# Optimization experiments

Measured on AMD Instinct MI355X. Metric: run time of the kernel, lower is better.

The kernel has to match this reference:

```python
import jax, jax.numpy as jnp
from jax import lax
import numpy as np

L, G, C = 4, 2, 4  # num_blocks, num_sparsity_groups, num_sparsity_cardinals
IMAGE_MEAN = 0.5
SCALE = 2


def _wn(v, g):
    # weight_norm over dims (1,2,3), g per output channel
    n = jnp.sqrt(jnp.sum(v * v, axis=(1, 2, 3), keepdims=True))
    return (g.reshape(-1, 1, 1, 1) / n) * v


def _conv(x, w, b, pad):
    y = lax.conv_general_dilated(x, w, (1, 1), [(pad, pad), (pad, pad)],
                                 dimension_numbers=('NCHW', 'OIHW', 'NCHW'))
    return y + b[None, :, None, None]


def _dyn_conv(x, v, g, b, mw, mb):
    # sparsity-routed conv: per-sample expert mixture of kernels
    w = _wn(v, g)                                   # [G*out, in, k, k]
    B = x.shape[0]
    logits = x.mean((-1, -2)) @ mw.T + mb           # [B, G*C]
    s = jax.nn.softmax(logits.reshape(B, G, C), axis=1)
    wv = w.reshape(G, C, -1, *w.shape[1:])          # [G, C, D, in, k, k]
    wper = jnp.einsum('bgc,gcdikl->bcdikl', s, wv)
    wper = wper.reshape(B, -1, *w.shape[1:])        # [B, out, in, k, k]
    bper = jnp.einsum('bgc,gcd->bcd', s, b.reshape(G, C, -1)).reshape(B, -1)

    def per_sample(xi, wi, bi):
        yi = lax.conv_general_dilated(xi[None], wi, (1, 1), [(1, 1), (1, 1)],
                                      dimension_numbers=('NCHW', 'OIHW', 'NCHW'))[0]
        return yi + bi[:, None, None]

    return jax.vmap(per_sample)(x, wper, bper)


def _pixel_shuffle(x, r):
    B, Cc, H, W = x.shape
    x = x.reshape(B, Cc // (r * r), r, r, H, W)
    x = x.transpose(0, 1, 4, 2, 5, 3)
    return x.reshape(B, Cc // (r * r), H * r, W * r)


def setup_inputs() -> dict:
    key = jax.random.key(0)
    ks = jax.random.split(key, 16)
    f32 = jnp.float32
    inp = {
        'x': jax.random.uniform(ks[0], (8, 3, 64, 64), dtype=f32),
        'head_v': jax.random.normal(ks[1], (64, 3, 3, 3), dtype=f32) * 0.05,
        'head_g': jnp.ones((64,), f32),
        'head_b': jnp.zeros((64,), f32),
        'b1_v': jax.random.normal(ks[2], (L, 512, 64, 3, 3), dtype=f32) * 0.05,
        'b1_g': jnp.full((L, 512), 2.0, f32),
        'b1_b': jnp.zeros((L, 512), f32),
        'b1_mw': jax.random.normal(ks[3], (L, 8, 64), dtype=f32) * 0.05,
        'b1_mb': jax.random.normal(ks[4], (L, 8), dtype=f32) * 0.05,
        'b2_v': jax.random.normal(ks[5], (L, 128, 256, 3, 3), dtype=f32) * 0.05,
        'b2_g': jnp.full((L, 128), 1.0 / np.sqrt(L), f32),
        'b2_b': jnp.zeros((L, 128), f32),
        'b2_mw': jax.random.normal(ks[6], (L, 8, 256), dtype=f32) * 0.05,
        'b2_mb': jax.random.normal(ks[7], (L, 8), dtype=f32) * 0.05,
        'tail_v': jax.random.normal(ks[8], (12, 64, 3, 3), dtype=f32) * 0.05,
        'tail_g': jnp.ones((12,), f32),
        'tail_b': jnp.zeros((12,), f32),
        'skip_v': jax.random.normal(ks[9], (12, 3, 5, 5), dtype=f32) * 0.05,
        'skip_g': jnp.ones((12,), f32),
        'skip_b': jnp.zeros((12,), f32),
    }
    return inp


def reference(x, head_v, head_g, head_b,
              b1_v, b1_g, b1_b, b1_mw, b1_mb,
              b2_v, b2_g, b2_b, b2_mw, b2_mb,
              tail_v, tail_g, tail_b,
              skip_v, skip_g, skip_b):
    x = x - IMAGE_MEAN
    h = _conv(x, _wn(head_v, head_g), head_b, pad=1)
    for l in range(L):
        r0 = h
        t = _dyn_conv(h, b1_v[l], b1_g[l], b1_b[l], b1_mw[l], b1_mb[l])
        t = jax.nn.relu(t)
        t = _dyn_conv(t, b2_v[l], b2_g[l], b2_b[l], b2_mw[l], b2_mb[l])
        h = t + r0
    body = _conv(h, _wn(tail_v, tail_g), tail_b, pad=1)
    s = _conv(x, _wn(skip_v, skip_g), skip_b, pad=2)
    y = _pixel_shuffle(body + s, SCALE) + IMAGE_MEAN
    return y
```

## Files before the change

kernel.cpp:

```cpp
#include <hip/hip_runtime.h>

typedef __attribute__((ext_vector_type(8))) short bf16x8;
typedef __attribute__((ext_vector_type(4))) float f32x4;
typedef __attribute__((ext_vector_type(4))) unsigned short u16x4;
typedef __attribute__((ext_vector_type(8))) unsigned short u16x8;

__device__ __forceinline__ unsigned short bf16u(float x) {
    unsigned int u = __builtin_bit_cast(unsigned int, x);
    unsigned int r = (u + 0x7fffu + ((u >> 16) & 1u)) >> 16;
    return (unsigned short)r;
}
__device__ __forceinline__ void gll16(const void* g, void* l) {
    __builtin_amdgcn_global_load_lds((const __attribute__((address_space(1))) void*)g,
                                     (__attribute__((address_space(3))) void*)l, 16, 0, 0);
}

__global__ __launch_bounds__(256) void zero_all(unsigned short* __restrict__ hbf,
                                                unsigned short* __restrict__ tbf,
                                                float* __restrict__ sums) {
    int i = blockIdx.x * 256 + threadIdx.x;
    u16x8 z8 = {0, 0, 0, 0, 0, 0, 0, 0};
    if (i < 16640) {
        int chv = i & 7, pb = i >> 3, pos = pb % 260, b = pb / 260;
        int y, x;
        if (pos < 66) { y = 0; x = pos; }
        else if (pos < 132) { y = 65; x = pos - 66; }
        else if (pos < 196) { y = pos - 131; x = 0; }
        else { y = pos - 195; x = 65; }
        *(u16x8*)&hbf[(((size_t)b * 66 + y) * 66 + x) * 64 + chv * 8] = z8;
    } else if (i < 83200) {
        int j = i - 16640;
        int chv = j & 31, pb = j >> 5, pos = pb % 260, b = pb / 260;
        int y, x;
        if (pos < 66) { y = 0; x = pos; }
        else if (pos < 132) { y = 65; x = pos - 66; }
        else if (pos < 196) { y = pos - 131; x = 0; }
        else { y = pos - 195; x = 65; }
        *(u16x8*)&tbf[(((size_t)b * 66 + y) * 66 + x) * 256 + chv * 8] = z8;
    } else {
        int k = i - 83200;
        f32x4 z4 = {0.f, 0.f, 0.f, 0.f};
        ((f32x4*)sums)[k] = z4;
    }
}

__global__ __launch_bounds__(256) void wn_all(
    const float* __restrict__ hv, const float* __restrict__ hg, float* __restrict__ hw,
    const float* __restrict__ tv, const float* __restrict__ tg, float* __restrict__ tw,
    const float* __restrict__ kv, const float* __restrict__ kg, float* __restrict__ kw,
    const float* __restrict__ b1v, const float* __restrict__ b1g, float* __restrict__ b1s,
    const float* __restrict__ b2v, const float* __restrict__ b2g, float* __restrict__ b2s) {
    int blk = blockIdx.x;
    const float *v, *g;
    float *outw = nullptr, *outs = nullptr;
    int len, row;
    if (blk < 64)        { v = hv;  g = hg;  outw = hw;  len = 27;   row = blk; }
    else if (blk < 76)   { v = tv;  g = tg;  outw = tw;  len = 576;  row = blk - 64; }
    else if (blk < 88)   { v = kv;  g = kg;  outw = kw;  len = 75;   row = blk - 76; }
    else if (blk < 2136) { v = b1v; g = b1g; outs = b1s; len = 576;  row = blk - 88; }
    else                 { v = b2v; g = b2g; outs = b2s; len = 2304; row = blk - 2136; }

    __shared__ float red[4];
    __shared__ float s_sc;
    const float* vr = v + (size_t)row * len;
    float ss = 0.f;
    for (int i = threadIdx.x; i < len; i += 256) { float a = vr[i]; ss += a * a; }
    for (int o = 32; o > 0; o >>= 1) ss += __shfl_down(ss, o);
    if ((threadIdx.x & 63) == 0) red[threadIdx.x >> 6] = ss;
    __syncthreads();
    if (threadIdx.x == 0) s_sc = g[row] / sqrtf(red[0] + red[1] + red[2] + red[3]);
    __syncthreads();
    float sc = s_sc;
    if (outs) {
        if (threadIdx.x == 0) outs[row] = sc;
    } else {
        float* orow = outw + (size_t)row * len;
        for (int i = threadIdx.x; i < len; i += 256) orow[i] = vr[i] * sc;
    }
}

__global__ __launch_bounds__(256) void combine_w2(
    const float* __restrict__ v, const float* __restrict__ scale,
    const float* __restrict__ msum, const float* __restrict__ mw,
    const float* __restrict__ mb, float* __restrict__ s_out,
    unsigned short* __restrict__ wq, int D, int IC, int OC, int MT, int icr) {
    __shared__ float lg[8];
    __shared__ float sv8[8];
    int tid = threadIdx.x;
    int bpb = (OC * IC * 9) >> 8;
    int b = blockIdx.x / bpb;
    {
        int j = tid >> 5, l32 = tid & 31;
        float part = 0.f;
        for (int i = l32; i < icr; i += 32) part += msum[b * icr + i] * mw[j * icr + i];
        for (int m = 16; m > 0; m >>= 1) part += __shfl_xor(part, m);
        if (l32 == 0) lg[j] = part * (1.f / 4096.f) + mb[j];
    }
    __syncthreads();
    if (tid < 8) {
        int g = tid >> 2, c = tid & 3;
        float l0 = lg[c], l1 = lg[4 + c];
        float m = fmaxf(l0, l1);
        float e0 = __expf(l0 - m), e1 = __expf(l1 - m);
        float val = ((g == 0) ? e0 : e1) / (e0 + e1);
        sv8[tid] = val;
        if (blockIdx.x == b * bpb) s_out[b * 8 + tid] = val;
    }
    __syncthreads();

    int idx = blockIdx.x * 256 + tid;
    int kj = idx & 7;
    int tmp = idx >> 3;
    int mo = tmp % MT; tmp /= MT;
    int kg = tmp & 3; tmp >>= 2;
    int t = tmp % 9; tmp /= 9;
    int KCh = IC >> 5;
    int kc = tmp % KCh; tmp /= KCh;
    int OT = OC / MT;
    int ot = tmp % OT;
    int oc = ot * MT + mo;
    int ic = kc * 32 + kg * 8 + kj;
    int c = oc / D;
    float s0 = sv8[c], s1 = sv8[4 + c];
    float val = s0 * scale[oc] * v[((size_t)oc * IC + ic) * 9 + t] +
                s1 * scale[OC + oc] * v[((size_t)(OC + oc) * IC + ic) * 9 + t];
    wq[idx] = bf16u(val);
}

__global__ void tail_repack(const float* __restrict__ tw, unsigned short* __restrict__ wq) {
    int idx = blockIdx.x * 256 + threadIdx.x;
    int kj = idx & 7;
    int tmp = idx >> 3;
    int mo = tmp % 16; tmp /= 16;
    int kg = tmp & 3; tmp >>= 2;
    int t = tmp % 9; tmp /= 9;
    int kc = tmp;
    int ic = kc * 32 + kg * 8 + kj;
    float val = (mo < 12) ? tw[((size_t)mo * 64 + ic) * 9 + t] : 0.f;
    wq[idx] = bf16u(val);
}

template <int IC, int OC, int MT, int WM, int WN, int NR,
          bool RELU, bool RES, bool WF32, bool WBF, int OCR, bool DYNB>
__global__ __launch_bounds__(256) void conv_mfma(
    const unsigned short* __restrict__ in_bf,
    const unsigned short* __restrict__ wq,
    const float* __restrict__ bias_raw, const float* __restrict__ s8, int lgD,
    const float* __restrict__ res, float* __restrict__ out,
    unsigned short* __restrict__ out_bf, float* __restrict__ msum, long wstride) {
    constexpr int KCH = IC / 32;
    constexpr int NRH = NR + 2;
    constexpr int NT = NR * 64;
    constexpr int NF = (NT / 16) / WN;
    constexpr int MW = MT / (16 * WM);
    constexpr int WELEM = 9 * 32 * MT;
    constexpr int SCH = NRH * 66 * 4;
    constexpr int WCH = WELEM / 8;

    __shared__ __align__(16) unsigned short S[NRH * 66 * 32];
    __shared__ __align__(16) unsigned short W[WELEM];
    __shared__ float MRED[WN][MT];

    const int b = blockIdx.z, ot = blockIdx.y;
    const int y0 = blockIdx.x * NR;
    const int tid = threadIdx.x;
    const int lane = tid & 63, wid = tid >> 6;
    const int wm = wid / WN, wn = wid % WN;
    const int l15 = lane & 15, lk = lane >> 4;
    const int wmo = wm * (MT / WM);
    const int wno = wn * (NT / WN);

    f32x4 acc[MW][NF];
#pragma unroll
    for (int mf = 0; mf < MW; ++mf)
#pragma unroll
        for (int nf = 0; nf < NF; ++nf)
#pragma unroll
            for (int q = 0; q < 4; ++q) acc[mf][nf][q] = 0.f;

    const unsigned short* inb = in_bf + (size_t)b * 66 * 66 * IC;
    const unsigned short* wqb = wq + (size_t)b * wstride + (size_t)ot * (KCH * WELEM);

    for (int kc = 0; kc < KCH; ++kc) {
        __syncthreads();
        const unsigned short* wsrc = wqb + kc * WELEM;
        for (int cb = wid; cb * 64 < WCH; cb += 4) {
            int p = cb * 64 + lane;
            if (p < WCH) gll16(wsrc + p * 8, (char*)W + p * 16);
        }
        const int icb = kc * 32;
        for (int cb = wid; cb * 64 < SCH; cb += 4) {
            int p = cb * 64 + lane;
            if (p < SCH) {
                int Lz = p ^ ((p >> 3) & 7);
                int lk2 = Lz & 3;
                int cr = Lz >> 2;
                int col = cr % 66, row = cr / 66;
                const unsigned short* src =
                    inb + ((size_t)(y0 + row) * 66 + col) * IC + icb + lk2 * 8;
                gll16(src, (char*)S + p * 16);
            }
        }
        __syncthreads();
#pragma unroll
        for (int t = 0; t < 9; ++t) {
            const int dy = t / 3, dx = t % 3;
            bf16x8 a[MW];
#pragma unroll
            for (int mf = 0; mf < MW; ++mf)
                a[mf] = *(const bf16x8*)&W[((t * 4 + lk) * MT + wmo + mf * 16 + l15) * 8];
#pragma unroll
            for (int nf = 0; nf < NF; ++nf) {
                int n = wno + nf * 16 + l15;
                int r = n >> 6, c = n & 63;
                int L = ((r + dy) * 66 + (c + dx)) * 4 + lk;
                int P = L ^ ((L >> 3) & 7);
                bf16x8 bv = *(const bf16x8*)((const char*)S + P * 16);
#pragma unroll
                for (int mf = 0; mf < MW; ++mf)
                    acc[mf][nf] = __builtin_amdgcn_mfma_f32_16x16x32_bf16(a[mf], bv, acc[mf][nf], 0, 0, 0);
            }
        }
    }

    float msr[MW][4];
#pragma unroll
    for (int mf = 0; mf < MW; ++mf) {
        int ocb = ot * MT + wmo + mf * 16 + lk * 4;
        float bv[4];
#pragma unroll
        for (int q = 0; q < 4; ++q) {
            int oc = ocb + q;
            bv[q] = 0.f;
            if (oc < OCR) {
                if (DYNB) {
                    int c = oc >> lgD;
                    bv[q] = s8[b * 8 + c] * bias_raw[oc] + s8[b * 8 + 4 + c] * bias_raw[OCR + oc];
                } else {
                    bv[q] = bias_raw[oc];
                }
            }
            msr[mf][q] = 0.f;
        }
#pragma unroll
        for (int nf = 0; nf < NF; ++nf) {
            int n = wno + nf * 16 + l15;
            int y = y0 + (n >> 6), x = n & 63;
            float vv[4];
#pragma unroll
            for (int q = 0; q < 4; ++q) {
                int oc = ocb + q;
                float v = 0.f;
                if (oc < OCR) {
                    v = acc[mf][nf][q] + bv[q];
                    if (RELU) v = fmaxf(v, 0.f);
                    size_t o = (((size_t)b * OCR + oc) * 64 + y) * 64 + x;
                    if (RES) v += res[o];
                    if (WF32) out[o] = v;
                    msr[mf][q] += v;
                }
                vv[q] = v;
            }
            if (WBF) {
                u16x4 pk;
#pragma unroll
                for (int q = 0; q < 4; ++q) pk[q] = bf16u(vv[q]);
                if (ocb < OCR)
                    *(u16x4*)&out_bf[(((size_t)b * 66 + y + 1) * 66 + (x + 1)) * OCR + ocb] = pk;
            }
        }
    }
    if (msum) {
#pragma unroll
        for (int mf = 0; mf < MW; ++mf)
#pragma unroll
            for (int q = 0; q < 4; ++q) {
                float vq = msr[mf][q];
                vq += __shfl_xor(vq, 1);
                vq += __shfl_xor(vq, 2);
                vq += __shfl_xor(vq, 4);
                vq += __shfl_xor(vq, 8);
                if (l15 == 0) MRED[wn][wmo + mf * 16 + lk * 4 + q] = vq;
            }
        __syncthreads();
        if (tid < MT) {
            float tot = 0.f;
#pragma unroll
            for (int w2 = 0; w2 < WN; ++w2) tot += MRED[w2][tid];
            atomicAdd(&msum[b * OCR + ot * MT + tid], tot);
        }
    }
}

__global__ __launch_bounds__(256) void head_conv(
    const float* __restrict__ in, const float* __restrict__ w,
    const float* __restrict__ bias, float* __restrict__ out,
    unsigned short* __restrict__ out_bf, float* __restrict__ hsum0) {
    constexpr int OCT = 16, IC = 3;
    __shared__ float s_in[34 * 34];
    __shared__ float s_w[OCT * 9];
    __shared__ float wred[4][OCT];
    int b = blockIdx.z;
    int ocBase = blockIdx.y * OCT;
    int ty0 = (blockIdx.x >> 1) * 32;
    int tx0 = (blockIdx.x & 1) * 32;
    int tid = threadIdx.x;
    int lane = tid & 63, wid = tid >> 6;
    int tx = tid & 15, ty = tid >> 4;

    float acc[OCT][4];
#pragma unroll
    for (int oc = 0; oc < OCT; ++oc)
#pragma unroll
        for (int p = 0; p < 4; ++p) acc[oc][p] = 0.f;

    const float* inb = in + (size_t)b * IC * 4096;
    for (int ic = 0; ic < IC; ++ic) {
        const float* src = inb + (size_t)ic * 4096;
        for (int i = tid; i < 34 * 34; i += 256) {
            int r = i / 34, cc = i % 34;
            int gy = ty0 + r - 1, gx = tx0 + cc - 1;
            float val = 0.f;
            if (gy >= 0 && gy < 64 && gx >= 0 && gx < 64) val = src[gy * 64 + gx] - 0.5f;
            s_in[i] = val;
        }
        for (int i = tid; i < OCT * 9; i += 256) {
            int oc = i / 9, t = i % 9;
            s_w[i] = w[((size_t)(ocBase + oc) * IC + ic) * 9 + t];
        }
        __syncthreads();
        float v[4][4];
#pragma unroll
        for (int r = 0; r < 4; ++r)
#pragma unroll
            for (int cc = 0; cc < 4; ++cc) v[r][cc] = s_in[(2 * ty + r) * 34 + (2 * tx + cc)];
#pragma unroll
        for (int oc = 0; oc < OCT; ++oc) {
#pragma unroll
            for (int ky = 0; ky < 3; ++ky)
#pragma unroll
                for (int kx = 0; kx < 3; ++kx) {
                    float wv = s_w[oc * 9 + ky * 3 + kx];
                    acc[oc][0] += wv * v[ky][kx];
                    acc[oc][1] += wv * v[ky][kx + 1];
                    acc[oc][2] += wv * v[ky + 1][kx];
                    acc[oc][3] += wv * v[ky + 1][kx + 1];
                }
        }
        __syncthreads();
    }
    int py = ty0 + 2 * ty, px = tx0 + 2 * tx;
#pragma unroll
    for (int oc = 0; oc < OCT; ++oc) {
        int og = ocBase + oc;
        float bv = bias[og];
        float osum = 0.f;
#pragma unroll
        for (int p = 0; p < 4; ++p) {
            int dy = p >> 1, dx = p & 1;
            float val = acc[oc][p] + bv;
            osum += val;
            out[(((size_t)b * 64 + og) * 64 + py + dy) * 64 + px + dx] = val;
            out_bf[(((size_t)b * 66 + py + dy + 1) * 66 + (px + dx + 1)) * 64 + og] = bf16u(val);
        }
        for (int m = 1; m < 64; m <<= 1) osum += __shfl_xor(osum, m);
        if (lane == 0) wred[wid][oc] = osum;
    }
    __syncthreads();
    if (tid < OCT)
        atomicAdd(&hsum0[b * 64 + ocBase + tid],
                  wred[0][tid] + wred[1][tid] + wred[2][tid] + wred[3][tid]);
}

__global__ __launch_bounds__(256) void shuffle_skip(
    const float* __restrict__ body, const float* __restrict__ x,
    const float* __restrict__ skw, const float* __restrict__ skb,
    float* __restrict__ out) {
    __shared__ float w[900];
    __shared__ float bb[12];
    int tid = threadIdx.x;
    for (int i = tid; i < 900; i += 256) w[i] = skw[i];
    if (tid < 12) bb[tid] = skb[tid];
    __syncthreads();
    int idx = blockIdx.x * 256 + tid;
    int ox = idx & 127;
    int oy = (idx >> 7) & 127;
    int v = idx >> 14;
    int c = v % 3;
    int b = v / 3;
    int rx = ox & 1, ry = oy & 1;
    int xx = ox >> 1, yy = oy >> 1;
    int ch = c * 4 + ry * 2 + rx;
    float acc = bb[ch];
    for (int ic = 0; ic < 3; ++ic)
        for (int ky = 0; ky < 5; ++ky) {
            int gy = yy + ky - 2;
            if (gy < 0 || gy >= 64) continue;
            for (int kx = 0; kx < 5; ++kx) {
                int gx = xx + kx - 2;
                if (gx < 0 || gx >= 64) continue;
                acc += w[((ch * 3 + ic) * 5 + ky) * 5 + kx] *
                       (x[((size_t)(b * 3 + ic) * 64 + gy) * 64 + gx] - 0.5f);
            }
        }
    size_t src = (((size_t)b * 12 + ch) * 64 + yy) * 64 + xx;
    out[idx] = body[src] + acc + 0.5f;
}

extern "C" void kernel_launch(void* const* d_in, const int* in_sizes, int n_in,
                              void* d_out, int out_size, void* d_ws, size_t ws_size,
                              hipStream_t stream) {
    const float* x      = (const float*)d_in[0];
    const float* head_v = (const float*)d_in[1];
    const float* head_g = (const float*)d_in[2];
    const float* head_b = (const float*)d_in[3];
    const float* b1_v   = (const float*)d_in[4];
    const float* b1_g   = (const float*)d_in[5];
    const float* b1_b   = (const float*)d_in[6];
    const float* b1_mw  = (const float*)d_in[7];
    const float* b1_mb  = (const float*)d_in[8];
    const float* b2_v   = (const float*)d_in[9];
    const float* b2_g   = (const float*)d_in[10];
    const float* b2_b   = (const float*)d_in[11];
    const float* b2_mw  = (const float*)d_in[12];
    const float* b2_mb  = (const float*)d_in[13];
    const float* tail_v = (const float*)d_in[14];
    const float* tail_g = (const float*)d_in[15];
    const float* tail_b = (const float*)d_in[16];
    const float* skip_v = (const float*)d_in[17];
    const float* skip_g = (const float*)d_in[18];
    const float* skip_b = (const float*)d_in[19];

    float* ws = (float*)d_ws;
    size_t off = 0;
    auto alloc = [&](size_t n) { float* p = ws + off; off += (n + 3) & ~(size_t)3; return p; };
    float* head_w = alloc(64 * 27);
    float* tail_w = alloc(12 * 576);
    float* skip_w = alloc(12 * 75);
    float* b1_sc  = alloc(2048);
    float* b2_sc  = alloc(512);
    float* h      = alloc((size_t)8 * 64 * 4096);
    float* sums   = alloc(10240);
    float* sbuf   = alloc(64);
    float* body   = alloc((size_t)8 * 12 * 4096);
    unsigned short* wq1  = (unsigned short*)alloc((size_t)8 * 256 * 576 / 2);
    unsigned short* wq2  = (unsigned short*)alloc((size_t)8 * 64 * 2304 / 2);
    unsigned short* wqt  = (unsigned short*)alloc(9216 / 2);
    unsigned short* h_bf = (unsigned short*)alloc((size_t)8 * 66 * 66 * 64 / 2);
    unsigned short* t_bf = (unsigned short*)alloc((size_t)8 * 66 * 66 * 256 / 2);
    (void)ws_size; (void)in_sizes; (void)n_in; (void)out_size;

    auto hsum = [&](int l) { return sums + l * 512; };
    auto tsum = [&](int l) { return sums + 2048 + l * 2048; };

    zero_all<<<335, 256, 0, stream>>>(h_bf, t_bf, sums);
    wn_all<<<2648, 256, 0, stream>>>(head_v, head_g, head_w, tail_v, tail_g, tail_w,
                                     skip_v, skip_g, skip_w, b1_v, b1_g, b1_sc,
                                     b2_v, b2_g, b2_sc);
    head_conv<<<dim3(4, 4, 8), 256, 0, stream>>>(x, head_w, head_b, h, h_bf, hsum(0));
    tail_repack<<<36, 256, 0, stream>>>(tail_w, wqt);

    for (int l = 0; l < 4; ++l) {
        combine_w2<<<4608, 256, 0, stream>>>(b1_v + (size_t)l * 512 * 576,
                                             b1_sc + (size_t)l * 512, hsum(l),
                                             b1_mw + (size_t)l * 8 * 64, b1_mb + l * 8,
                                             sbuf, wq1, 64, 64, 256, 64, 64);
        conv_mfma<64, 256, 64, 1, 4, 4, true, false, false, true, 256, true>
            <<<dim3(16, 4, 8), 256, 0, stream>>>(h_bf, wq1, b1_b + (size_t)l * 512, sbuf, 6,
                                                 nullptr, nullptr, t_bf, tsum(l), 147456);
        combine_w2<<<4608, 256, 0, stream>>>(b2_v + (size_t)l * 128 * 2304,
                                             b2_sc + (size_t)l * 128, tsum(l),
                                             b2_mw + (size_t)l * 8 * 256, b2_mb + l * 8,
                                             sbuf, wq2, 16, 256, 64, 32, 256);
        conv_mfma<256, 64, 32, 2, 2, 2, false, true, true, true, 64, true>
            <<<dim3(32, 2, 8), 256, 0, stream>>>(t_bf, wq2, b2_b + (size_t)l * 128, sbuf, 4,
                                                 h, h, h_bf, (l < 3) ? hsum(l + 1) : nullptr,
                                                 147456);
    }

    conv_mfma<64, 16, 16, 1, 4, 4, false, false, true, false, 12, false>
        <<<dim3(16, 1, 8), 256, 0, stream>>>(h_bf, wqt, tail_b, nullptr, 0,
                                             nullptr, body, nullptr, nullptr, 0);
    shuffle_skip<<<1536, 256, 0, stream>>>(body, x, skip_w, skip_b, (float*)d_out);
}
```

Before: 351.1 us.

## Double-buffer conv staging, block activations by 64 channels, rewrite weight combine

The conv kernel now stages the next K-chunk of weights and inputs into a second LDS buffer while the current chunk feeds the MFMAs, leaving one barrier per chunk instead of two. Intermediate activations are stored as 64-channel blocks so each K-chunk reads a compact region. The weight-combine kernel caches the needed weight rows in shared memory and writes packed 8-element bf16 vectors instead of one scalar per thread. The second conv uses a 64-channel output tile with one tile in the OC dimension. The cost is roughly double LDS use, which lowers occupancy, and fewer blocks for the second conv.

```diff
diff --git a/kernel.cpp b/kernel.cpp
--- a/kernel.cpp
+++ b/kernel.cpp
@@ -30,13 +30,14 @@
         *(u16x8*)&hbf[(((size_t)b * 66 + y) * 66 + x) * 64 + chv * 8] = z8;
     } else if (i < 83200) {
         int j = i - 16640;
-        int chv = j & 31, pb = j >> 5, pos = pb % 260, b = pb / 260;
+        int chv = j & 7, pb = j >> 3;
+        int pos = pb % 260, bc = pb / 260;
         int y, x;
         if (pos < 66) { y = 0; x = pos; }
         else if (pos < 132) { y = 65; x = pos - 66; }
         else if (pos < 196) { y = pos - 131; x = 0; }
         else { y = pos - 195; x = 65; }
-        *(u16x8*)&tbf[(((size_t)b * 66 + y) * 66 + x) * 256 + chv * 8] = z8;
+        *(u16x8*)&tbf[(((size_t)bc * 66 + y) * 66 + x) * 64 + chv * 8] = z8;
     } else {
         int k = i - 83200;
         f32x4 z4 = {0.f, 0.f, 0.f, 0.f};
@@ -79,22 +80,30 @@
     }
 }
 
-__global__ __launch_bounds__(256) void combine_w2(
+template <int IC, int GOC, int LGG>
+__global__ __launch_bounds__(256) void combine_v2(
     const float* __restrict__ v, const float* __restrict__ scale,
     const float* __restrict__ msum, const float* __restrict__ mw,
     const float* __restrict__ mb, float* __restrict__ s_out,
-    unsigned short* __restrict__ wq, int D, int IC, int OC, int MT, int icr) {
-    __shared__ float lg[8];
-    __shared__ float sv8[8];
+    unsigned short* __restrict__ wq, int D, int OC) {
+    constexpr int ROWF = IC * 9;
+    constexpr int KCh = IC / 32;
+    constexpr int TOTC = GOC * KCh * 9 * 4;
+    __shared__ float lv[2 * GOC * ROWF];
+    __shared__ float lg[8], sv8[8];
     int tid = threadIdx.x;
-    int bpb = (OC * IC * 9) >> 8;
-    int b = blockIdx.x / bpb;
+    int b = blockIdx.y, ocg = blockIdx.x * GOC;
     {
         int j = tid >> 5, l32 = tid & 31;
         float part = 0.f;
-        for (int i = l32; i < icr; i += 32) part += msum[b * icr + i] * mw[j * icr + i];
+        for (int i = l32; i < IC; i += 32) part += msum[b * IC + i] * mw[j * IC + i];
         for (int m = 16; m > 0; m >>= 1) part += __shfl_xor(part, m);
         if (l32 == 0) lg[j] = part * (1.f / 4096.f) + mb[j];
+    }
+    for (int i = tid; i < 2 * GOC * ROWF; i += 256) {
+        int r = i / ROWF, jj = i - r * ROWF;
+        int oc_r = (r / GOC) * OC + ocg + (r % GOC);
+        lv[i] = v[(size_t)oc_r * ROWF + jj] * scale[oc_r];
     }
     __syncthreads();
     if (tid < 8) {
@@ -104,27 +113,29 @@
         float e0 = __expf(l0 - m), e1 = __expf(l1 - m);
         float val = ((g == 0) ? e0 : e1) / (e0 + e1);
         sv8[tid] = val;
-        if (blockIdx.x == b * bpb) s_out[b * 8 + tid] = val;
-    }
-    __syncthreads();
-
-    int idx = blockIdx.x * 256 + tid;
-    int kj = idx & 7;
-    int tmp = idx >> 3;
-    int mo = tmp % MT; tmp /= MT;
-    int kg = tmp & 3; tmp >>= 2;
-    int t = tmp % 9; tmp /= 9;
-    int KCh = IC >> 5;
-    int kc = tmp % KCh; tmp /= KCh;
-    int OT = OC / MT;
-    int ot = tmp % OT;
-    int oc = ot * MT + mo;
-    int ic = kc * 32 + kg * 8 + kj;
-    int c = oc / D;
-    float s0 = sv8[c], s1 = sv8[4 + c];
-    float val = s0 * scale[oc] * v[((size_t)oc * IC + ic) * 9 + t] +
-                s1 * scale[OC + oc] * v[((size_t)(OC + oc) * IC + ic) * 9 + t];
-    wq[idx] = bf16u(val);
+        if (blockIdx.x == 0) s_out[b * 8 + tid] = val;
+    }
+    __syncthreads();
+    for (int ci = tid; ci < TOTC; ci += 256) {
+        int ml = ci & (GOC - 1);
+        int c = ci >> LGG;
+        int kg = c & 3, c2 = c >> 2;
+        int t = c2 % 9, kc = c2 / 9;
+        int oc = ocg + ml;
+        int cd = oc / D;
+        float s0 = sv8[cd], s1 = sv8[4 + cd];
+        const float* p0 = &lv[(size_t)ml * ROWF];
+        const float* p1 = &lv[(size_t)(GOC + ml) * ROWF];
+        u16x8 pk;
+#pragma unroll
+        for (int kj = 0; kj < 8; ++kj) {
+            int ic9 = (kc * 32 + kg * 8 + kj) * 9 + t;
+            pk[kj] = bf16u(s0 * p0[ic9] + s1 * p1[ic9]);
+        }
+        int ot = oc >> 6, mo = oc & 63;
+        size_t w_off = ((((size_t)(b * (OC >> 6) + ot) * KCh + kc) * 9 + t) * 4 + kg) * 512 + mo * 8;
+        *(u16x8*)&wq[w_off] = pk;
+    }
 }
 
 __global__ void tail_repack(const float* __restrict__ tw, unsigned short* __restrict__ wq) {
@@ -154,17 +165,20 @@
     constexpr int NF = (NT / 16) / WN;
     constexpr int MW = MT / (16 * WM);
     constexpr int WELEM = 9 * 32 * MT;
-    constexpr int SCH = NRH * 66 * 4;
+    constexpr int SELEM = NRH * 66 * 32;
     constexpr int WCH = WELEM / 8;
-
-    __shared__ __align__(16) unsigned short S[NRH * 66 * 32];
-    __shared__ __align__(16) unsigned short W[WELEM];
+    constexpr int SCH = SELEM / 8;
+    constexpr int OCB = (OCR % 64 == 0) ? OCR / 64 : 1;
+
+    __shared__ __align__(16) unsigned short S[2][SELEM];
+    __shared__ __align__(16) unsigned short W[2][WELEM];
     __shared__ float MRED[WN][MT];
 
     const int b = blockIdx.z, ot = blockIdx.y;
     const int y0 = blockIdx.x * NR;
     const int tid = threadIdx.x;
-    const int lane = tid & 63, wid = tid >> 6;
+    const int lane = tid & 63;
+    const int wid = tid >> 6;
     const int wm = wid / WN, wn = wid % WN;
     const int l15 = lane & 15, lk = lane >> 4;
     const int wmo = wm * (MT / WM);
@@ -178,49 +192,49 @@
 #pragma unroll
             for (int q = 0; q < 4; ++q) acc[mf][nf][q] = 0.f;
 
-    const unsigned short* inb = in_bf + (size_t)b * 66 * 66 * IC;
+    const unsigned short* inb = in_bf + (size_t)b * (IC / 64) * 4356 * 64;
     const unsigned short* wqb = wq + (size_t)b * wstride + (size_t)ot * (KCH * WELEM);
 
+    auto STAGE = [&](int kc, int buf) {
+        const unsigned short* wsrc = wqb + (size_t)kc * WELEM;
+        for (int i = tid; i < WCH; i += 256)
+            gll16(wsrc + i * 8, (char*)W[buf] + i * 16);
+        const unsigned short* sb = inb + (size_t)(kc >> 1) * (4356 * 64) + (kc & 1) * 32;
+        for (int i = tid; i < SCH; i += 256) {
+            int Lz = i ^ ((i >> 3) & 7);
+            int lk2 = Lz & 3, cr = Lz >> 2;
+            int col = cr % 66, row = cr / 66;
+            gll16(sb + ((size_t)(y0 + row) * 66 + col) * 64 + lk2 * 8,
+                  (char*)S[buf] + i * 16);
+        }
+    };
+
+    STAGE(0, 0);
+    __syncthreads();
     for (int kc = 0; kc < KCH; ++kc) {
-        __syncthreads();
-        const unsigned short* wsrc = wqb + kc * WELEM;
-        for (int cb = wid; cb * 64 < WCH; cb += 4) {
-            int p = cb * 64 + lane;
-            if (p < WCH) gll16(wsrc + p * 8, (char*)W + p * 16);
-        }
-        const int icb = kc * 32;
-        for (int cb = wid; cb * 64 < SCH; cb += 4) {
-            int p = cb * 64 + lane;
-            if (p < SCH) {
-                int Lz = p ^ ((p >> 3) & 7);
-                int lk2 = Lz & 3;
-                int cr = Lz >> 2;
-                int col = cr % 66, row = cr / 66;
-                const unsigned short* src =
-                    inb + ((size_t)(y0 + row) * 66 + col) * IC + icb + lk2 * 8;
-                gll16(src, (char*)S + p * 16);
-            }
-        }
-        __syncthreads();
+        if (kc + 1 < KCH) STAGE(kc + 1, (kc + 1) & 1);
+        const unsigned short* Sb = S[kc & 1];
+        const unsigned short* Wb = W[kc & 1];
 #pragma unroll
         for (int t = 0; t < 9; ++t) {
             const int dy = t / 3, dx = t % 3;
             bf16x8 a[MW];
 #pragma unroll
             for (int mf = 0; mf < MW; ++mf)
-                a[mf] = *(const bf16x8*)&W[((t * 4 + lk) * MT + wmo + mf * 16 + l15) * 8];
+                a[mf] = *(const bf16x8*)&Wb[((t * 4 + lk) * MT + wmo + mf * 16 + l15) * 8];
 #pragma unroll
             for (int nf = 0; nf < NF; ++nf) {
                 int n = wno + nf * 16 + l15;
                 int r = n >> 6, c = n & 63;
                 int L = ((r + dy) * 66 + (c + dx)) * 4 + lk;
                 int P = L ^ ((L >> 3) & 7);
-                bf16x8 bv = *(const bf16x8*)((const char*)S + P * 16);
+                bf16x8 bv = *(const bf16x8*)((const char*)Sb + P * 16);
 #pragma unroll
                 for (int mf = 0; mf < MW; ++mf)
                     acc[mf][nf] = __builtin_amdgcn_mfma_f32_16x16x32_bf16(a[mf], bv, acc[mf][nf], 0, 0, 0);
             }
         }
+        __syncthreads();
     }
 
     float msr[MW][4];
@@ -266,7 +280,8 @@
 #pragma unroll
                 for (int q = 0; q < 4; ++q) pk[q] = bf16u(vv[q]);
                 if (ocb < OCR)
-                    *(u16x4*)&out_bf[(((size_t)b * 66 + y + 1) * 66 + (x + 1)) * OCR + ocb] = pk;
+                    *(u16x4*)&out_bf[((((size_t)b * OCB + (ocb >> 6)) * 66 + y + 1) * 66 +
+                                      (x + 1)) * 64 + (ocb & 63)] = pk;
             }
         }
     }
@@ -447,7 +462,7 @@
     unsigned short* wq2  = (unsigned short*)alloc((size_t)8 * 64 * 2304 / 2);
     unsigned short* wqt  = (unsigned short*)alloc(9216 / 2);
     unsigned short* h_bf = (unsigned short*)alloc((size_t)8 * 66 * 66 * 64 / 2);
-    unsigned short* t_bf = (unsigned short*)alloc((size_t)8 * 66 * 66 * 256 / 2);
+    unsigned short* t_bf = (unsigned short*)alloc((size_t)8 * 4 * 66 * 66 * 64 / 2);
     (void)ws_size; (void)in_sizes; (void)n_in; (void)out_size;
 
     auto hsum = [&](int l) { return sums + l * 512; };
@@ -461,19 +476,17 @@
     tail_repack<<<36, 256, 0, stream>>>(tail_w, wqt);
 
     for (int l = 0; l < 4; ++l) {
-        combine_w2<<<4608, 256, 0, stream>>>(b1_v + (size_t)l * 512 * 576,
-                                             b1_sc + (size_t)l * 512, hsum(l),
-                                             b1_mw + (size_t)l * 8 * 64, b1_mb + l * 8,
-                                             sbuf, wq1, 64, 64, 256, 64, 64);
+        combine_v2<64, 4, 2><<<dim3(64, 8), 256, 0, stream>>>(
+            b1_v + (size_t)l * 512 * 576, b1_sc + (size_t)l * 512, hsum(l),
+            b1_mw + (size_t)l * 8 * 64, b1_mb + l * 8, sbuf, wq1, 64, 256);
         conv_mfma<64, 256, 64, 1, 4, 4, true, false, false, true, 256, true>
             <<<dim3(16, 4, 8), 256, 0, stream>>>(h_bf, wq1, b1_b + (size_t)l * 512, sbuf, 6,
                                                  nullptr, nullptr, t_bf, tsum(l), 147456);
-        combine_w2<<<4608, 256, 0, stream>>>(b2_v + (size_t)l * 128 * 2304,
-                                             b2_sc + (size_t)l * 128, tsum(l),
-                                             b2_mw + (size_t)l * 8 * 256, b2_mb + l * 8,
-                                             sbuf, wq2, 16, 256, 64, 32, 256);
-        conv_mfma<256, 64, 32, 2, 2, 2, false, true, true, true, 64, true>
-            <<<dim3(32, 2, 8), 256, 0, stream>>>(t_bf, wq2, b2_b + (size_t)l * 128, sbuf, 4,
+        combine_v2<256, 2, 1><<<dim3(32, 8), 256, 0, stream>>>(
+            b2_v + (size_t)l * 128 * 2304, b2_sc + (size_t)l * 128, tsum(l),
+            b2_mw + (size_t)l * 8 * 256, b2_mb + l * 8, sbuf, wq2, 16, 64);
+        conv_mfma<256, 64, 64, 2, 2, 2, false, true, true, true, 64, true>
+            <<<dim3(32, 1, 8), 256, 0, stream>>>(t_bf, wq2, b2_b + (size_t)l * 128, sbuf, 4,
                                                  h, h, h_bf, (l < 3) ? hsum(l + 1) : nullptr,
                                                  147456);
     }
```

Measured after the change: 365.6 us. 1.04x slower.
